# Kernel tuning notes

Hardware: AMD Instinct MI355X
Metric: run time of the kernel (lower is better)

Reference implementation:

```python
import jax, jax.numpy as jnp
import numpy as np

D_MODEL = 512
NHEAD = 4
HEAD_DIM = D_MODEL // NHEAD


def setup_inputs() -> dict:
    key = jax.random.key(0)
    ks = jax.random.split(key, 12)
    B, S = 2, 4096
    s = 1.0 / np.sqrt(D_MODEL)
    inp = {
        "query": jax.random.normal(ks[0], (B, S, D_MODEL), jnp.float32),
        "key": jax.random.normal(ks[1], (B, S, D_MODEL), jnp.float32),
        "value": jax.random.normal(ks[2], (B, S, D_MODEL), jnp.float32),
        "Wq": jax.random.uniform(ks[3], (D_MODEL, D_MODEL), jnp.float32, -s, s),
        "bq": jax.random.uniform(ks[4], (D_MODEL,), jnp.float32, -s, s),
        "Wk": jax.random.uniform(ks[5], (D_MODEL, D_MODEL), jnp.float32, -s, s),
        "bk": jax.random.uniform(ks[6], (D_MODEL,), jnp.float32, -s, s),
        "Wv": jax.random.uniform(ks[7], (D_MODEL, D_MODEL), jnp.float32, -s, s),
        "bv": jax.random.uniform(ks[8], (D_MODEL,), jnp.float32, -s, s),
        "Wo": jax.random.uniform(ks[9], (D_MODEL, D_MODEL), jnp.float32, -s, s),
        "bo": jax.random.uniform(ks[10], (D_MODEL,), jnp.float32, -s, s),
    }
    return inp


def reference(query, key, value, Wq, bq, Wk, bk, Wv, bv, Wo, bo):
    B, Sq, _ = query.shape
    Sk = key.shape[1]
    # projections (torch Linear: x @ W.T + b); split heads -> [B, H, S, hd]
    def proj(x, W, b, S):
        return (x @ W.T + b).reshape(B, S, NHEAD, HEAD_DIM).transpose(0, 2, 1, 3)
    Q = proj(query, Wq, bq, Sq)
    K = proj(key, Wk, bk, Sk)
    V = proj(value, Wv, bv, Sk)
    scale = 1.0 / np.sqrt(HEAD_DIM).astype(np.float32)
    scores = jnp.einsum("bhqd,bhkd->bhqk", Q, K) * scale  # [B,H,Sq,Sk]
    weights = jax.nn.softmax(scores, axis=-1)
    out = jnp.einsum("bhqk,bhkd->bhqd", weights, V)  # [B,H,Sq,hd]
    out = out.transpose(0, 2, 1, 3).reshape(B, Sq, D_MODEL)
    return out @ Wo.T + bo
```

## Files before the change

### kernel.cpp

```cpp
#include <hip/hip_runtime.h>


#define D_MODEL 512
#define NHEAD 4
#define HD 128
#define S_ 4096

typedef __attribute__((ext_vector_type(8))) short bf16x8;
typedef __attribute__((ext_vector_type(4))) short bf16x4;
typedef __attribute__((ext_vector_type(4))) float f32x4;
typedef __attribute__((ext_vector_type(2))) unsigned uint2v;
typedef __attribute__((ext_vector_type(4))) unsigned uint4v;

#define SCQ (0.08838834764831845f * 1.4426950408889634f)

__device__ __forceinline__ short f2bf(float f) {
    unsigned u = __builtin_bit_cast(unsigned, f);
    u += 0x7fffu + ((u >> 16) & 1u);
    return (short)(u >> 16);
}
__device__ __forceinline__ unsigned pk2bf(float a, float b) {
    unsigned ua = __builtin_bit_cast(unsigned, a);
    ua += 0x7fffu + ((ua >> 16) & 1u);
    unsigned ub = __builtin_bit_cast(unsigned, b);
    ub += 0x7fffu + ((ub >> 16) & 1u);
    return (ua >> 16) | (ub & 0xffff0000u);
}
__device__ __forceinline__ void gl2lds16(const short* g, short* l) {
    __builtin_amdgcn_global_load_lds(
        (const __attribute__((address_space(1))) void*)g,
        (__attribute__((address_space(3))) void*)l, 16, 0, 0);
}

__global__ __launch_bounds__(256) void convert_kernel(
    const float* __restrict__ s0, const float* __restrict__ s1,
    const float* __restrict__ s2, const float* __restrict__ s3,
    const float* __restrict__ s4, const float* __restrict__ s5,
    const float* __restrict__ s6,
    short* __restrict__ d0, short* __restrict__ d1, short* __restrict__ d2,
    short* __restrict__ d3, short* __restrict__ d4, short* __restrict__ d5,
    short* __restrict__ d6)
{
    int seg = blockIdx.y;
    const float* src; short* dst; int n;
    const int NBIG = 2 * S_ * D_MODEL;
    const int NW = D_MODEL * D_MODEL;
    switch (seg) {
        case 0: src = s0; dst = d0; n = NBIG; break;
        case 1: src = s1; dst = d1; n = NBIG; break;
        case 2: src = s2; dst = d2; n = NBIG; break;
        case 3: src = s3; dst = d3; n = NW; break;
        case 4: src = s4; dst = d4; n = NW; break;
        case 5: src = s5; dst = d5; n = NW; break;
        default: src = s6; dst = d6; n = NW; break;
    }
    int idx = (blockIdx.x * 256 + threadIdx.x) * 8;
    if (idx >= n) return;
    float4 a = *(const float4*)(src + idx);
    float4 b = *(const float4*)(src + idx + 4);
    uint4v o;
    o[0] = pk2bf(a.x, a.y); o[1] = pk2bf(a.z, a.w);
    o[2] = pk2bf(b.x, b.y); o[3] = pk2bf(b.z, b.w);
    *(uint4v*)(dst + idx) = o;
}

__global__ __launch_bounds__(256) void qkv_kernel(
    const short* __restrict__ qb, const short* __restrict__ kb,
    const short* __restrict__ vb,
    const short* __restrict__ Wqb, const short* __restrict__ Wkb,
    const short* __restrict__ Wvb,
    const float* __restrict__ bq, const float* __restrict__ bk,
    const float* __restrict__ bv,
    short* __restrict__ Qh, short* __restrict__ Kh, short* __restrict__ VT)
{
    __shared__ short smem[12288];
    short* lA = smem;
    short* lB = smem + 4096;
    int z = blockIdx.z;
    const short* A    = (z == 0) ? qb  : (z == 1) ? kb  : vb;
    const short* W    = (z == 0) ? Wqb : (z == 1) ? Wkb : Wvb;
    const float* bias = (z == 0) ? bq  : (z == 1) ? bk  : bv;
    short* out        = (z == 0) ? Qh  : (z == 1) ? Kh  : VT;
    int vmode = (z == 2);
    float osc = (z == 0) ? SCQ : 1.0f;

    int t = threadIdx.x;
    int wv = t >> 6, ln = t & 63, q4 = ln >> 4, c = ln & 15;
    int m0 = blockIdx.x * 64, n0 = blockIdx.y * 128;
    f32x4 acc[8] = {};

    for (int k0 = 0; k0 < 512; k0 += 64) {
        for (int i = 0; i < 2; ++i) {
            int id = i * 256 + t;
            int m = id >> 3, kgp = id & 7;
            gl2lds16(A + (size_t)(m0 + m) * 512 + k0 + ((kgp ^ (m & 7)) << 3),
                     &lA[id * 8]);
        }
        for (int i = 0; i < 4; ++i) {
            int id = i * 256 + t;
            int n = id >> 3, kgp = id & 7;
            gl2lds16(W + (size_t)(n0 + n) * 512 + k0 + ((kgp ^ (n & 7)) << 3),
                     &lB[id * 8]);
        }
        __syncthreads();
        for (int ks = 0; ks < 2; ++ks) {
            int kg = ks * 4 + q4;
            int m = wv * 16 + c;
            bf16x8 af = *(bf16x8*)&lA[m * 64 + ((kg ^ (m & 7)) << 3)];
            bf16x8 bfr[8];
            for (int nt = 0; nt < 8; ++nt) {
                int n = nt * 16 + c;
                bfr[nt] = *(bf16x8*)&lB[n * 64 + ((kg ^ (n & 7)) << 3)];
            }
            for (int nt = 0; nt < 8; ++nt)
                acc[nt] = __builtin_amdgcn_mfma_f32_16x16x32_bf16(af, bfr[nt], acc[nt], 0, 0, 0);
        }
        __syncthreads();
    }

    if (vmode == 0) {
        const int TS = 136;
        short* lT = smem;
        for (int nt = 0; nt < 8; ++nt) {
            float bv_ = bias[n0 + nt * 16 + c];
            for (int r = 0; r < 4; ++r) {
                int srow = wv * 16 + q4 * 4 + r;
                lT[srow * TS + nt * 16 + c] = f2bf((acc[nt][r] + bv_) * osc);
            }
        }
        __syncthreads();
        int bb = m0 >> 12, sbase = m0 & 4095, h = blockIdx.y;
        for (int i = 0; i < 4; ++i) {
            int id = i * 256 + t;
            int row = id >> 4, g = id & 15;
            bf16x8 vv = *(bf16x8*)&lT[row * TS + g * 8];
            *(bf16x8*)&out[((size_t)((bb * NHEAD + h) * S_ + sbase + row)) * HD + g * 8] = vv;
        }
    } else {
        for (int nt = 0; nt < 8; ++nt) {
            int d = nt * 16 + c;
            float bv_ = bias[n0 + d];
            uint2v pv;
            pv[0] = pk2bf(acc[nt][0] + bv_, acc[nt][1] + bv_);
            pv[1] = pk2bf(acc[nt][2] + bv_, acc[nt][3] + bv_);
            int gr = wv * 4 + q4;
            *(uint2v*)&lB[d * 64 + ((gr ^ (d & 15)) << 2)] = pv;
        }
        __syncthreads();
        int bb = m0 >> 12, sbase = m0 & 4095, h = blockIdx.y;
        for (int i = 0; i < 8; ++i) {
            int id = i * 256 + t;
            int d = id >> 4, grl = id & 15;
            bf16x4 v = *(bf16x4*)&lB[d * 64 + ((grl ^ (d & 15)) << 2)];
            *(bf16x4*)&out[((size_t)((bb * NHEAD + h) * HD + d)) * S_ + sbase + grl * 4] = v;
        }
    }
}

__global__ __launch_bounds__(256) void outproj_kernel(
    const short* __restrict__ A, const short* __restrict__ W,
    const float* __restrict__ bias, float* __restrict__ out)
{
    __shared__ short lA[64 * 64];
    __shared__ short lB[128 * 64];
    int t = threadIdx.x;
    int wv = t >> 6, ln = t & 63, q4 = ln >> 4, c = ln & 15;
    int m0 = blockIdx.x * 64, n0 = blockIdx.y * 128;
    f32x4 acc[8] = {};

    for (int k0 = 0; k0 < 512; k0 += 64) {
        for (int i = 0; i < 2; ++i) {
            int id = i * 256 + t;
            int m = id >> 3, kgp = id & 7;
            gl2lds16(A + (size_t)(m0 + m) * 512 + k0 + ((kgp ^ (m & 7)) << 3),
                     &lA[id * 8]);
        }
        for (int i = 0; i < 4; ++i) {
            int id = i * 256 + t;
            int n = id >> 3, kgp = id & 7;
            gl2lds16(W + (size_t)(n0 + n) * 512 + k0 + ((kgp ^ (n & 7)) << 3),
                     &lB[id * 8]);
        }
        __syncthreads();
        for (int ks = 0; ks < 2; ++ks) {
            int kg = ks * 4 + q4;
            int m = wv * 16 + c;
            bf16x8 af = *(bf16x8*)&lA[m * 64 + ((kg ^ (m & 7)) << 3)];
            bf16x8 bfr[8];
            for (int nt = 0; nt < 8; ++nt) {
                int n = nt * 16 + c;
                bfr[nt] = *(bf16x8*)&lB[n * 64 + ((kg ^ (n & 7)) << 3)];
            }
            for (int nt = 0; nt < 8; ++nt)
                acc[nt] = __builtin_amdgcn_mfma_f32_16x16x32_bf16(af, bfr[nt], acc[nt], 0, 0, 0);
        }
        __syncthreads();
    }

    for (int nt = 0; nt < 8; ++nt) {
        int col = n0 + nt * 16 + c;
        float bv_ = bias[col];
        for (int r = 0; r < 4; ++r) {
            int mrow = m0 + wv * 16 + q4 * 4 + r;
            out[(size_t)mrow * 512 + col] = acc[nt][r] + bv_;
        }
    }
}

__global__ __launch_bounds__(256, 2) void flash_kernel(
    const short* __restrict__ Qh, const short* __restrict__ Kh,
    const short* __restrict__ VTg, short* __restrict__ AO,
    float* __restrict__ U, float* __restrict__ ML, int nsplit, int kkspan)
{
    __shared__ short lK[2][64 * 128];
    __shared__ short lVT[128 * 64];
    __shared__ short lP[128 * 64];
    int t = threadIdx.x;
    int wv = t >> 6, ln = t & 63, q4 = ln >> 4, c = ln & 15;
    int bh = blockIdx.x;
    int s0 = blockIdx.y * 128;
    int z = blockIdx.z;
    const size_t base = (size_t)bh * S_ * HD;

    bf16x8 qf[2][4];
    #pragma unroll
    for (int qt = 0; qt < 2; ++qt) {
        int s = s0 + wv * 32 + qt * 16 + c;
        const short* qp = Qh + base + (size_t)s * HD + q4 * 8;
        #pragma unroll
        for (int ks = 0; ks < 4; ++ks)
            qf[qt][ks] = *(const bf16x8*)(qp + ks * 32);
    }

    f32x4 of[8][2] = {};
    float lrun[2] = {};

    int kkbeg = z * kkspan;
    int nt = kkspan >> 6;

    #pragma unroll
    for (int i = 0; i < 4; ++i) {
        int id = i * 256 + t;
        int m = id >> 4, kgp = id & 15;
        gl2lds16(Kh + base + (size_t)(kkbeg + m) * HD + ((kgp ^ (m & 7)) << 3),
                 &lK[0][id * 8]);
    }
    #pragma unroll
    for (int i = 0; i < 4; ++i) {
        int id = i * 256 + t;
        int mv = id >> 3, kgvp = id & 7;
        gl2lds16(VTg + base + (size_t)mv * S_ + kkbeg + ((kgvp ^ (mv & 7)) << 3),
                 &lVT[id * 8]);
    }
    asm volatile("s_waitcnt vmcnt(4)" ::: "memory");
    __builtin_amdgcn_s_barrier();
    __builtin_amdgcn_sched_barrier(0);

    int cur = 0;
    for (int it = 0; it < nt; ++it) {
        int kk0 = kkbeg + it * 64;
        int more = (it + 1 < nt);

        if (more) {
            #pragma unroll
            for (int i = 0; i < 4; ++i) {
                int id = i * 256 + t;
                int m = id >> 4, kgp = id & 15;
                gl2lds16(Kh + base + (size_t)(kk0 + 64 + m) * HD + ((kgp ^ (m & 7)) << 3),
                         &lK[cur ^ 1][id * 8]);
            }
        }

        f32x4 sf[2][4] = {};
        __builtin_amdgcn_s_setprio(1);
        #pragma unroll
        for (int ks = 0; ks < 4; ++ks) {
            int kg = ks * 4 + q4;
            bf16x8 af[4];
            #pragma unroll
            for (int kt = 0; kt < 4; ++kt) {
                int row = kt * 16 + c;
                af[kt] = *(bf16x8*)&lK[cur][row * 128 + ((kg ^ (row & 7)) << 3)];
            }
            #pragma unroll
            for (int qt = 0; qt < 2; ++qt)
                #pragma unroll
                for (int kt = 0; kt < 4; ++kt)
                    sf[qt][kt] = __builtin_amdgcn_mfma_f32_16x16x32_bf16(
                        af[kt], qf[qt][ks], sf[qt][kt], 0, 0, 0);
        }
        __builtin_amdgcn_s_setprio(0);

        #pragma unroll
        for (int qt = 0; qt < 2; ++qt) {
            float lt = 0.f;
            int row = wv * 32 + qt * 16 + c;
            #pragma unroll
            for (int kt = 0; kt < 4; ++kt) {
                float p0 = exp2f(sf[qt][kt][0]);
                float p1 = exp2f(sf[qt][kt][1]);
                float p2 = exp2f(sf[qt][kt][2]);
                float p3 = exp2f(sf[qt][kt][3]);
                lt += (p0 + p1) + (p2 + p3);
                uint2v pv;
                pv[0] = pk2bf(p0, p1);
                pv[1] = pk2bf(p2, p3);
                int g = kt * 2 + (q4 >> 1);
                *(uint2v*)&lP[row * 64 + ((g ^ (row & 7)) << 3) + ((q4 & 1) << 2)] = pv;
            }
            lt += __shfl_xor(lt, 16);
            lt += __shfl_xor(lt, 32);
            lrun[qt] += lt;
        }

        if (more) asm volatile("s_waitcnt vmcnt(4)" ::: "memory");
        else      asm volatile("s_waitcnt vmcnt(0)" ::: "memory");
        __builtin_amdgcn_s_barrier();
        __builtin_amdgcn_sched_barrier(0);

        __builtin_amdgcn_s_setprio(1);
        #pragma unroll
        for (int ksv = 0; ksv < 2; ++ksv) {
            int kg = ksv * 4 + q4;
            bf16x8 av[8], bp[2];
            #pragma unroll
            for (int dt = 0; dt < 8; ++dt) {
                int row = dt * 16 + c;
                av[dt] = *(bf16x8*)&lVT[row * 64 + ((kg ^ (row & 7)) << 3)];
            }
            #pragma unroll
            for (int qt = 0; qt < 2; ++qt) {
                int row = wv * 32 + qt * 16 + c;
                bp[qt] = *(bf16x8*)&lP[row * 64 + ((kg ^ (row & 7)) << 3)];
            }
            #pragma unroll
            for (int qt = 0; qt < 2; ++qt)
                #pragma unroll
                for (int dt = 0; dt < 8; ++dt)
                    of[dt][qt] = __builtin_amdgcn_mfma_f32_16x16x32_bf16(
                        av[dt], bp[qt], of[dt][qt], 0, 0, 0);
        }
        __builtin_amdgcn_s_setprio(0);

        asm volatile("s_waitcnt vmcnt(0)" ::: "memory");
        __builtin_amdgcn_s_barrier();
        __builtin_amdgcn_sched_barrier(0);

        if (more) {
            #pragma unroll
            for (int i = 0; i < 4; ++i) {
                int id = i * 256 + t;
                int mv = id >> 3, kgvp = id & 7;
                gl2lds16(VTg + base + (size_t)mv * S_ + kk0 + 64 + ((kgvp ^ (mv & 7)) << 3),
                         &lVT[id * 8]);
            }
        }
        cur ^= 1;
    }

    if (nsplit > 1) {
        #pragma unroll
        for (int qt = 0; qt < 2; ++qt) {
            int s = s0 + wv * 32 + qt * 16 + c;
            size_t rowu = (size_t)(z * 8 + bh) * S_ + s;
            float* up = U + rowu * HD;
            #pragma unroll
            for (int dt = 0; dt < 8; ++dt)
                *(f32x4*)&up[dt * 16 + q4 * 4] = of[dt][qt];
            if (q4 == 0) ML[rowu] = lrun[qt];
        }
    } else {
        int b = bh >> 2, h = bh & 3;
        #pragma unroll
        for (int qt = 0; qt < 2; ++qt) {
            float inv = 1.0f / lrun[qt];
            int s = s0 + wv * 32 + qt * 16 + c;
            short* dst = AO + ((size_t)(b * S_ + s)) * D_MODEL + h * HD;
            #pragma unroll
            for (int dt = 0; dt < 8; ++dt) {
                uint2v ov;
                ov[0] = pk2bf(of[dt][qt][0] * inv, of[dt][qt][1] * inv);
                ov[1] = pk2bf(of[dt][qt][2] * inv, of[dt][qt][3] * inv);
                *(uint2v*)(dst + dt * 16 + q4 * 4) = ov;
            }
        }
    }
}

__global__ __launch_bounds__(256) void combine_kernel(
    const float* __restrict__ U, const float* __restrict__ ML,
    short* __restrict__ AO, int nsplit)
{
    int row = blockIdx.x * 8 + (threadIdx.x >> 5);
    int d4 = (threadIdx.x & 31) * 4;
    const int R = 8 * S_;
    float l = 0.f;
    f32x4 u = {0.f, 0.f, 0.f, 0.f};
    for (int zz = 0; zz < nsplit; ++zz) {
        l += ML[(size_t)zz * R + row];
        f32x4 uz = *(const f32x4*)&U[((size_t)zz * R + row) * HD + d4];
        u += uz;
    }
    float inv = 1.0f / l;
    uint2v o;
    o[0] = pk2bf(u[0] * inv, u[1] * inv);
    o[1] = pk2bf(u[2] * inv, u[3] * inv);
    int bh = row >> 12, s = row & 4095;
    int b = bh >> 2, h = bh & 3;
    *(uint2v*)&AO[((size_t)(b * S_ + s)) * D_MODEL + h * HD + d4] = o;
}

extern "C" void kernel_launch(void* const* d_in, const int* in_sizes, int n_in,
                              void* d_out, int out_size, void* d_ws, size_t ws_size,
                              hipStream_t stream) {
    const float* q  = (const float*)d_in[0];
    const float* k  = (const float*)d_in[1];
    const float* v  = (const float*)d_in[2];
    const float* Wq = (const float*)d_in[3];
    const float* bq = (const float*)d_in[4];
    const float* Wk = (const float*)d_in[5];
    const float* bk = (const float*)d_in[6];
    const float* Wv = (const float*)d_in[7];
    const float* bv = (const float*)d_in[8];
    const float* Wo = (const float*)d_in[9];
    const float* bo = (const float*)d_in[10];

    const size_t HS = (size_t)2 * NHEAD * S_ * HD;
    const size_t NBIG = HS;
    const size_t NW = (size_t)D_MODEL * D_MODEL;
    const size_t R = (size_t)8 * S_;

    char* wsb = (char*)d_ws;
    short* Qh = (short*)wsb;
    short* Kh = Qh + HS;
    short* VT = Kh + HS;
    short* AO = VT + HS;
    char* r2 = wsb + 4 * HS * 2;
    short* qb  = (short*)r2;
    short* kb  = qb + NBIG;
    short* vb  = kb + NBIG;
    short* Wqb = vb + NBIG;
    short* Wkb = Wqb + NW;
    short* Wvb = Wkb + NW;
    float* U   = (float*)r2;

    int nsplit = 1;
    size_t r2sz = 3 * NBIG * 2 + 3 * NW * 2;
    for (int cand = 4; cand >= 2; cand -= 2) {
        size_t r2c = (size_t)cand * R * HD * 4;
        if (r2c < 3 * NBIG * 2 + 3 * NW * 2) r2c = 3 * NBIG * 2 + 3 * NW * 2;
        size_t need = 4 * HS * 2 + r2c + (size_t)cand * R * 4 + NW * 2;
        if (ws_size >= need) { nsplit = cand; r2sz = r2c; break; }
    }
    float* ML  = (float*)(r2 + r2sz);
    short* Wob = (short*)((char*)ML + (size_t)nsplit * R * 4);
    int kkspan = S_ / nsplit;

    dim3 blk(256);
    convert_kernel<<<dim3(2048, 7), blk, 0, stream>>>(
        q, k, v, Wq, Wk, Wv, Wo, qb, kb, vb, Wqb, Wkb, Wvb, Wob);
    qkv_kernel<<<dim3(128, 4, 3), blk, 0, stream>>>(
        qb, kb, vb, Wqb, Wkb, Wvb, bq, bk, bv, Qh, Kh, VT);
    flash_kernel<<<dim3(8, 32, nsplit), blk, 0, stream>>>(
        Qh, Kh, VT, AO, U, ML, nsplit, kkspan);
    if (nsplit > 1)
        combine_kernel<<<dim3(S_), blk, 0, stream>>>(U, ML, AO, nsplit);
    outproj_kernel<<<dim3(128, 4), blk, 0, stream>>>(AO, Wob, bo, (float*)d_out);
}
```

Baseline: 249.0 us.

## Keep softmax probabilities in registers via permlane swaps instead of LDS staging

Drops the shared-memory P buffer. Probabilities are packed with v_cvt_pk_bf16_f32 and rearranged into the MFMA B-operand layout with permlane32/permlane16 swap instructions, so the LDS write and read-back of P disappear. The per-iteration row-sum cross-lane shuffles move out of the loop and run once at the end. The smaller LDS footprint allows raising launch bounds to 3 blocks per SM, which tightens the register budget and risks spills.

```diff
diff --git a/kernel.cpp b/kernel.cpp
--- a/kernel.cpp
+++ b/kernel.cpp
@@ -207,14 +207,13 @@
     }
 }
 
-__global__ __launch_bounds__(256, 2) void flash_kernel(
+__global__ __launch_bounds__(256, 3) void flash_kernel(
     const short* __restrict__ Qh, const short* __restrict__ Kh,
     const short* __restrict__ VTg, short* __restrict__ AO,
     float* __restrict__ U, float* __restrict__ ML, int nsplit, int kkspan)
 {
     __shared__ short lK[2][64 * 128];
     __shared__ short lVT[128 * 64];
-    __shared__ short lP[128 * 64];
     int t = threadIdx.x;
     int wv = t >> 6, ln = t & 63, q4 = ln >> 4, c = ln & 15;
     int bh = blockIdx.x;
@@ -291,10 +290,11 @@
         }
         __builtin_amdgcn_s_setprio(0);
 
+        bf16x8 bp[2][2];
         #pragma unroll
         for (int qt = 0; qt < 2; ++qt) {
+            unsigned dlo[4], dhi[4];
             float lt = 0.f;
-            int row = wv * 32 + qt * 16 + c;
             #pragma unroll
             for (int kt = 0; kt < 4; ++kt) {
                 float p0 = exp2f(sf[qt][kt][0]);
@@ -302,15 +302,21 @@
                 float p2 = exp2f(sf[qt][kt][2]);
                 float p3 = exp2f(sf[qt][kt][3]);
                 lt += (p0 + p1) + (p2 + p3);
-                uint2v pv;
-                pv[0] = pk2bf(p0, p1);
-                pv[1] = pk2bf(p2, p3);
-                int g = kt * 2 + (q4 >> 1);
-                *(uint2v*)&lP[row * 64 + ((g ^ (row & 7)) << 3) + ((q4 & 1) << 2)] = pv;
-            }
-            lt += __shfl_xor(lt, 16);
-            lt += __shfl_xor(lt, 32);
+                asm("v_cvt_pk_bf16_f32 %0, %1, %2" : "=v"(dlo[kt]) : "v"(p0), "v"(p1));
+                asm("v_cvt_pk_bf16_f32 %0, %1, %2" : "=v"(dhi[kt]) : "v"(p2), "v"(p3));
+            }
             lrun[qt] += lt;
+            #pragma unroll
+            for (int ksv = 0; ksv < 2; ++ksv) {
+                unsigned x0 = dlo[2 * ksv], y0 = dlo[2 * ksv + 1];
+                unsigned x1 = dhi[2 * ksv], y1 = dhi[2 * ksv + 1];
+                asm("v_permlane32_swap_b32 %0, %1" : "+v"(x0), "+v"(y0));
+                asm("v_permlane16_swap_b32 %0, %1" : "+v"(x0), "+v"(y0));
+                asm("v_permlane32_swap_b32 %0, %1" : "+v"(x1), "+v"(y1));
+                asm("v_permlane16_swap_b32 %0, %1" : "+v"(x1), "+v"(y1));
+                uint4v u; u[0] = x0; u[1] = x1; u[2] = y0; u[3] = y1;
+                bp[qt][ksv] = __builtin_bit_cast(bf16x8, u);
+            }
         }
 
         if (more) asm volatile("s_waitcnt vmcnt(4)" ::: "memory");
@@ -322,23 +328,18 @@
         #pragma unroll
         for (int ksv = 0; ksv < 2; ++ksv) {
             int kg = ksv * 4 + q4;
-            bf16x8 av[8], bp[2];
+            bf16x8 av[8];
             #pragma unroll
             for (int dt = 0; dt < 8; ++dt) {
                 int row = dt * 16 + c;
                 av[dt] = *(bf16x8*)&lVT[row * 64 + ((kg ^ (row & 7)) << 3)];
-            }
-            #pragma unroll
-            for (int qt = 0; qt < 2; ++qt) {
-                int row = wv * 32 + qt * 16 + c;
-                bp[qt] = *(bf16x8*)&lP[row * 64 + ((kg ^ (row & 7)) << 3)];
             }
             #pragma unroll
             for (int qt = 0; qt < 2; ++qt)
                 #pragma unroll
                 for (int dt = 0; dt < 8; ++dt)
                     of[dt][qt] = __builtin_amdgcn_mfma_f32_16x16x32_bf16(
-                        av[dt], bp[qt], of[dt][qt], 0, 0, 0);
+                        av[dt], bp[qt][ksv], of[dt][qt], 0, 0, 0);
         }
         __builtin_amdgcn_s_setprio(0);
 
@@ -356,6 +357,12 @@
             }
         }
         cur ^= 1;
+    }
+
+    #pragma unroll
+    for (int qt = 0; qt < 2; ++qt) {
+        lrun[qt] += __shfl_xor(lrun[qt], 16);
+        lrun[qt] += __shfl_xor(lrun[qt], 32);
     }
 
     if (nsplit > 1) {
```

New measurement: 406.1 us. 63.1% more time.
